# Optimization experiments

Measured on AMD Instinct MI355X. Metric: run time of the kernel, lower is better.

The kernel has to match this reference:

```python
import jax, jax.numpy as jnp
import numpy as np

N_NODES = 100000
N_EDGES = 1600000
IN_DIM = 256
HID_DIM = 64
NUM_CLASSES = 32
NEG_SLOPE = 0.01  # F.leaky_relu default


def setup_inputs() -> dict:
    key = jax.random.key(0)
    k1, k2, k3, k4, k5, k6 = jax.random.split(key, 6)
    return {
        "local_features": jax.random.normal(k1, (N_NODES, IN_DIM), dtype=jnp.float32),
        "edge_index": jax.random.randint(k2, (2, N_EDGES), 0, N_NODES, dtype=jnp.int64),
        "weight1": jax.random.uniform(k3, (IN_DIM, HID_DIM), dtype=jnp.float32),
        "weight2": jax.random.uniform(k4, (HID_DIM, NUM_CLASSES), dtype=jnp.float32),
        "att_weight1": jax.random.uniform(k5, (2 * HID_DIM, 1), dtype=jnp.float32),
        "att_weight2": jax.random.uniform(k6, (2 * NUM_CLASSES, 1), dtype=jnp.float32),
    }


def _gat_attention_aggregate(H, a, src, dst, n_nodes):
    # H: [N, D], a: [2D, 1]. Edge score = leaky_relu([H_src||H_dst] @ a)
    # computed without materializing [E, 2D]: split a into src/dst halves.
    d = H.shape[1]
    s_score = (H @ a[:d]).squeeze(-1)   # [N]
    d_score = (H @ a[d:]).squeeze(-1)   # [N]
    e = jax.nn.leaky_relu(s_score[src] + d_score[dst], NEG_SLOPE)  # [E]
    # segment softmax over each row (grouped by src), as torch.sparse.softmax(dim=1)
    m = jax.ops.segment_max(e, src, num_segments=n_nodes)          # [N]
    ex = jnp.exp(e - m[src])                                       # [E]
    denom = jax.ops.segment_sum(ex, src, num_segments=n_nodes)     # [N]
    att = ex / denom[src]                                          # [E]
    # sparse mm: out[i] = sum_{(i,j) in E} att_ij * H[j]
    return jax.ops.segment_sum(att[:, None] * H[dst], src, num_segments=n_nodes)


def reference(local_features, edge_index, weight1, weight2, att_weight1, att_weight2):
    src, dst = edge_index[0], edge_index[1]
    n = local_features.shape[0]
    Hw1 = local_features @ weight1                                  # [N, HID]
    hidden = jax.nn.elu(_gat_attention_aggregate(Hw1, att_weight1, src, dst, n))
    Hw2 = hidden @ weight2                                          # [N, C]
    out = _gat_attention_aggregate(Hw2, att_weight2, src, dst, n)
    return jax.nn.log_softmax(out, axis=1)
```

## Files before the change

kernel.cpp:

```cpp
#include <hip/hip_runtime.h>
#include <math.h>

#define IN_DIM 256
#define HID 64
#define NC 32
#define NEG 0.01f
#define INF_NEG -1e30f
#define SXR 68
#define MAXNBK 512
#define SLOT 8256
#define BCAP 12288
#define BIN_CHUNK 8192

static inline int ceil_div(int a, int b){ return (a + b - 1) / b; }

static __device__ __forceinline__ float lrelu(float x){ return x > 0.f ? x : NEG * x; }


__global__ __launch_bounds__(256) void bin_kernel(const int* __restrict__ src,
      const int* __restrict__ dst, int* __restrict__ cursor,
      unsigned int* __restrict__ tmp, int E, int nbk){
  __shared__ unsigned int payload[BIN_CHUNK];
  __shared__ unsigned short bid[BIN_CHUNK];
  __shared__ int cnt[MAXNBK];
  __shared__ int lofs[MAXNBK];
  __shared__ int gbase[MAXNBK];
  __shared__ int s2[256];
  int tid = threadIdx.x;
  int beg = blockIdx.x * BIN_CHUNK;
  int end = min(E, beg + BIN_CHUNK);
  int len = end - beg;

  for (int i = tid; i < MAXNBK; i += 256) cnt[i] = 0;
  __syncthreads();
  for (int e = beg + tid; e < end; e += 256)
    atomicAdd(&cnt[src[e] >> 8], 1);
  __syncthreads();
  int a0 = cnt[2 * tid], a1 = cnt[2 * tid + 1];
  int pair = a0 + a1;
  s2[tid] = pair; __syncthreads();
  int val = pair;
  for (int off = 1; off < 256; off <<= 1){
    int add = (tid >= off) ? s2[tid - off] : 0;
    __syncthreads();
    val += add; s2[tid] = val;
    __syncthreads();
  }
  int ep = val - pair;
  lofs[2 * tid] = ep;
  lofs[2 * tid + 1] = ep + a0;
  __syncthreads();
  for (int i = tid; i < nbk; i += 256){
    int c = cnt[i];
    gbase[i] = (c > 0) ? atomicAdd(&cursor[i], c) : 0;
  }
  __syncthreads();
  for (int i = tid; i < MAXNBK; i += 256) cnt[i] = 0;
  __syncthreads();
  for (int e = beg + tid; e < end; e += 256){
    int s = src[e];
    int b = s >> 8;
    int r = atomicAdd(&cnt[b], 1);
    int pos = lofs[b] + r;
    payload[pos] = ((unsigned)(s & 255) << 17) | (unsigned)dst[e];
    bid[pos] = (unsigned short)b;
  }
  __syncthreads();
  for (int pos = tid; pos < len; pos += 256){
    int b = bid[pos];
    int idx = pos - lofs[b];
    int g = gbase[b] + idx;
    if (g < SLOT) tmp[(size_t)b * SLOT + g] = payload[pos];
  }
}

__global__ __launch_bounds__(512) void bucket_base_kernel(const int* __restrict__ cursor,
      int* __restrict__ bbase, int nbk){
  __shared__ int sh[512];
  int tid = threadIdx.x;
  int v = (tid < nbk) ? min(cursor[tid], SLOT) : 0;
  sh[tid] = v; __syncthreads();
  int val = v;
  for (int off = 1; off < 512; off <<= 1){
    int add = (tid >= off) ? sh[tid - off] : 0;
    __syncthreads();
    val += add; sh[tid] = val;
    __syncthreads();
  }
  if (tid < nbk) bbase[tid] = val - v;
}

__global__ __launch_bounds__(256) void bucket_scatter_kernel(const unsigned int* __restrict__ tmp,
      const int* __restrict__ cursor, const int* __restrict__ bbase,
      int* __restrict__ row_ptr, int* __restrict__ csr, int n){
  __shared__ int cnt[256];
  __shared__ int cur[256];
  __shared__ int lbuf[BCAP];
  int tid = threadIdx.x;
  int b = blockIdx.x;
  int n0 = b << 8;
  int nn = min(256, n - n0);
  int len = min(cursor[b], SLOT);
  int segb = bbase[b];
  const unsigned int* T = tmp + (size_t)b * SLOT;
  cnt[tid] = 0;
  __syncthreads();
  for (int e = tid; e < len; e += 256) atomicAdd(&cnt[T[e] >> 17], 1);
  __syncthreads();
  int tv = cnt[tid];
  int val = tv;
  for (int off = 1; off < 256; off <<= 1){
    int add = (tid >= off) ? cnt[tid - off] : 0;
    __syncthreads();
    val += add; cnt[tid] = val;
    __syncthreads();
  }
  int excl = val - tv;
  cur[tid] = excl;
  if (tid < nn) row_ptr[n0 + tid] = segb + excl;
  if (n0 + nn == n && tid == 0) row_ptr[n] = segb + len;
  __syncthreads();
  if (len <= BCAP){
    for (int e = tid; e < len; e += 256){
      unsigned v = T[e];
      int pos = atomicAdd(&cur[v >> 17], 1);
      lbuf[pos] = (int)(v & 0x1FFFF);
    }
    __syncthreads();
    for (int e = tid; e < len; e += 256) csr[segb + e] = lbuf[e];
  } else {
    for (int e = tid; e < len; e += 256){
      unsigned v = T[e];
      int pos = atomicAdd(&cur[v >> 17], 1);
      csr[segb + pos] = (int)(v & 0x1FFFF);
    }
  }
}


__global__ void hist_kernel(const int* __restrict__ src, int* __restrict__ counts, int E){
  int i = blockIdx.x * blockDim.x + threadIdx.x;
  if (i < E) atomicAdd(&counts[src[i]], 1);
}
__global__ void scan_blocks_kernel(const int* __restrict__ counts, int* __restrict__ excl,
                                   int* __restrict__ bsums, int n){
  __shared__ int sh[256];
  int tid = threadIdx.x;
  int base = blockIdx.x * 1024 + tid * 4;
  int c[4]; int tsum = 0;
  #pragma unroll
  for (int j = 0; j < 4; j++){ int i = base + j; c[j] = (i < n) ? counts[i] : 0; tsum += c[j]; }
  sh[tid] = tsum; __syncthreads();
  int val = tsum;
  for (int off = 1; off < 256; off <<= 1){
    int add = (tid >= off) ? sh[tid - off] : 0;
    __syncthreads();
    val += add; sh[tid] = val;
    __syncthreads();
  }
  int p = val - tsum;
  #pragma unroll
  for (int j = 0; j < 4; j++){ int i = base + j; if (i < n) excl[i] = p; p += c[j]; }
  if (tid == 255) bsums[blockIdx.x] = val;
}
__global__ void scan_sums_kernel(int* __restrict__ bsums, int* __restrict__ row_ptr,
                                 int nb, int n, int E){
  __shared__ int sh[256];
  int tid = threadIdx.x;
  int v = (tid < nb) ? bsums[tid] : 0;
  sh[tid] = v; __syncthreads();
  int val = v;
  for (int off = 1; off < 256; off <<= 1){
    int add = (tid >= off) ? sh[tid - off] : 0;
    __syncthreads();
    val += add; sh[tid] = val;
    __syncthreads();
  }
  if (tid < nb) bsums[tid] = val - v;
  if (tid == 0) row_ptr[n] = E;
}
__global__ void add_offsets_kernel(int* __restrict__ excl, const int* __restrict__ bsums, int n){
  int i = blockIdx.x * 1024 + threadIdx.x;
  if (i < n) excl[i] += bsums[blockIdx.x];
}
__global__ void scatter_kernel(const int* __restrict__ src, const int* __restrict__ dst,
                               const int* __restrict__ row_ptr, int* __restrict__ fill,
                               int* __restrict__ csr, int E){
  int i = blockIdx.x * blockDim.x + threadIdx.x;
  if (i >= E) return;
  int s = src[i];
  int pos = row_ptr[s] + atomicAdd(&fill[s], 1);
  csr[pos] = dst[i];
}


__global__ __launch_bounds__(256) void gemm1_kernel(const float* __restrict__ X, const float* __restrict__ W,
      const float* __restrict__ a, float* __restrict__ H,
      float* __restrict__ svec, float* __restrict__ dvec, int n){
  __shared__ float xs[128 * SXR];
  __shared__ float ws[64 * 64];
  int tid = threadIdx.x;
  int r0 = blockIdx.x * 128;
  int tr = tid >> 4;
  int tc = tid & 15;
  int srow = tid >> 4, sc4 = tid & 15;

  float4 pfx[8], pfw[4];
  #pragma unroll
  for (int p = 0; p < 8; p++){
    int row = p * 16 + srow;
    int gr = r0 + row;
    pfx[p] = make_float4(0.f, 0.f, 0.f, 0.f);
    if (gr < n) pfx[p] = *(const float4*)(X + (size_t)gr * IN_DIM + sc4 * 4);
  }
  #pragma unroll
  for (int p = 0; p < 4; p++){
    int k = p * 16 + srow;
    pfw[p] = *(const float4*)(W + (size_t)k * 64 + sc4 * 4);
  }

  float acc[8][4];
  #pragma unroll
  for (int i = 0; i < 8; i++)
    #pragma unroll
    for (int j = 0; j < 4; j++) acc[i][j] = 0.f;

  for (int kb = 0; kb < 4; kb++){
    __syncthreads();
    #pragma unroll
    for (int p = 0; p < 8; p++){
      int row = p * 16 + srow;
      *(float4*)(xs + row * SXR + sc4 * 4) = pfx[p];
    }
    #pragma unroll
    for (int p = 0; p < 4; p++){
      int k = p * 16 + srow;
      *(float4*)(ws + k * 64 + sc4 * 4) = pfw[p];
    }
    if (kb < 3){
      #pragma unroll
      for (int p = 0; p < 8; p++){
        int row = p * 16 + srow;
        int gr = r0 + row;
        pfx[p] = make_float4(0.f, 0.f, 0.f, 0.f);
        if (gr < n) pfx[p] = *(const float4*)(X + (size_t)gr * IN_DIM + (kb + 1) * 64 + sc4 * 4);
      }
      #pragma unroll
      for (int p = 0; p < 4; p++){
        int k = p * 16 + srow;
        pfw[p] = *(const float4*)(W + (size_t)((kb + 1) * 64 + k) * 64 + sc4 * 4);
      }
    }
    __syncthreads();
    for (int kq = 0; kq < 16; kq++){
      float xr[8][4];
      #pragma unroll
      for (int i = 0; i < 8; i++){
        float4 v = *(const float4*)(xs + (tr * 8 + i) * SXR + kq * 4);
        xr[i][0] = v.x; xr[i][1] = v.y; xr[i][2] = v.z; xr[i][3] = v.w;
      }
      #pragma unroll
      for (int dk = 0; dk < 4; dk++){
        float4 w4 = *(const float4*)(ws + (size_t)(kq * 4 + dk) * 64 + tc * 4);
        float wv[4] = {w4.x, w4.y, w4.z, w4.w};
        #pragma unroll
        for (int i = 0; i < 8; i++)
          #pragma unroll
          for (int j = 0; j < 4; j++) acc[i][j] = fmaf(xr[i][dk], wv[j], acc[i][j]);
      }
    }
  }

  float av[4], bv[4];
  #pragma unroll
  for (int j = 0; j < 4; j++){ av[j] = a[tc * 4 + j]; bv[j] = a[64 + tc * 4 + j]; }
  float sp[8], dp[8];
  #pragma unroll
  for (int i = 0; i < 8; i++){
    float s = 0.f, d = 0.f;
    #pragma unroll
    for (int j = 0; j < 4; j++){ s = fmaf(acc[i][j], av[j], s); d = fmaf(acc[i][j], bv[j], d); }
    sp[i] = s; dp[i] = d;
  }
  #pragma unroll
  for (int off = 1; off < 16; off <<= 1){
    #pragma unroll
    for (int i = 0; i < 8; i++){
      sp[i] += __shfl_xor(sp[i], off, 16);
      dp[i] += __shfl_xor(dp[i], off, 16);
    }
  }
  #pragma unroll
  for (int i = 0; i < 8; i++){
    int r = r0 + tr * 8 + i;
    if (r < n){
      *(float4*)(H + (size_t)r * 64 + tc * 4) = make_float4(acc[i][0], acc[i][1], acc[i][2], acc[i][3]);
      if (tc == 0){ svec[r] = sp[i]; dvec[r] = dp[i]; }
    }
  }
}


__global__ __launch_bounds__(256) void gemm2_kernel(const float* __restrict__ X, const float* __restrict__ W,
      const float* __restrict__ a, float* __restrict__ H,
      float* __restrict__ svec, float* __restrict__ dvec, int n){
  __shared__ float xs[128 * SXR];
  __shared__ float ws[64 * 32];
  int tid = threadIdx.x;
  int r0 = blockIdx.x * 128;
  int tr = tid >> 4;
  int tc = tid & 15;
  int srow = tid >> 4, sc4 = tid & 15;

  #pragma unroll
  for (int p = 0; p < 8; p++){
    int row = p * 16 + srow;
    int gr = r0 + row;
    float4 v = make_float4(0.f, 0.f, 0.f, 0.f);
    if (gr < n) v = *(const float4*)(X + (size_t)gr * HID + sc4 * 4);
    *(float4*)(xs + row * SXR + sc4 * 4) = v;
  }
  #pragma unroll
  for (int p = 0; p < 2; p++){
    int idx = p * 256 + tid;
    int k = idx >> 3, c4 = idx & 7;
    *(float4*)(ws + k * 32 + c4 * 4) = *(const float4*)(W + (size_t)k * 32 + c4 * 4);
  }
  __syncthreads();

  float acc[8][2];
  #pragma unroll
  for (int i = 0; i < 8; i++){ acc[i][0] = 0.f; acc[i][1] = 0.f; }

  for (int kq = 0; kq < 16; kq++){
    float xr[8][4];
    #pragma unroll
    for (int i = 0; i < 8; i++){
      float4 v = *(const float4*)(xs + (tr * 8 + i) * SXR + kq * 4);
      xr[i][0] = v.x; xr[i][1] = v.y; xr[i][2] = v.z; xr[i][3] = v.w;
    }
    #pragma unroll
    for (int dk = 0; dk < 4; dk++){
      float2 w2 = *(const float2*)(ws + (size_t)(kq * 4 + dk) * 32 + tc * 2);
      #pragma unroll
      for (int i = 0; i < 8; i++){
        acc[i][0] = fmaf(xr[i][dk], w2.x, acc[i][0]);
        acc[i][1] = fmaf(xr[i][dk], w2.y, acc[i][1]);
      }
    }
  }

  float a0 = a[tc * 2], a1 = a[tc * 2 + 1];
  float b0 = a[32 + tc * 2], b1 = a[32 + tc * 2 + 1];
  float sp[8], dp[8];
  #pragma unroll
  for (int i = 0; i < 8; i++){
    sp[i] = fmaf(acc[i][0], a0, acc[i][1] * a1);
    dp[i] = fmaf(acc[i][0], b0, acc[i][1] * b1);
  }
  #pragma unroll
  for (int off = 1; off < 16; off <<= 1){
    #pragma unroll
    for (int i = 0; i < 8; i++){
      sp[i] += __shfl_xor(sp[i], off, 16);
      dp[i] += __shfl_xor(dp[i], off, 16);
    }
  }
  #pragma unroll
  for (int i = 0; i < 8; i++){
    int r = r0 + tr * 8 + i;
    if (r < n){
      *(float2*)(H + (size_t)r * NC + tc * 2) = make_float2(acc[i][0], acc[i][1]);
      if (tc == 0){ svec[r] = sp[i]; dvec[r] = dp[i]; }
    }
  }
}


__global__ __launch_bounds__(256) void agg1_kernel(const float* __restrict__ H, const float* __restrict__ sv,
      const float* __restrict__ dv, const int* __restrict__ row_ptr, const int* __restrict__ csr,
      float* __restrict__ out, int n){
  int t = blockIdx.x * 256 + threadIdx.x;
  int g = t >> 4, fl = t & 15;
  if (g >= n) return;
  int beg = row_ptr[g], end = row_ptr[g + 1];
  float si = sv[g];
  float m = INF_NEG, l = 0.f;
  float ox = 0.f, oy = 0.f, oz = 0.f, ow = 0.f;

  for (int cb = beg; cb < end; cb += 32){
    int ce = min(cb + 32, end);
    int e0 = cb + fl, e1 = cb + 16 + fl;
    int d0 = 0, d1 = 0;
    float ev0 = INF_NEG, ev1 = INF_NEG;
    if (e0 < ce){ d0 = csr[e0]; ev0 = lrelu(si + dv[d0]); }
    if (e1 < ce){ d1 = csr[e1]; ev1 = lrelu(si + dv[d1]); }
    float lm = fmaxf(ev0, ev1);
    #pragma unroll
    for (int off = 1; off < 16; off <<= 1) lm = fmaxf(lm, __shfl_xor(lm, off, 16));
    float nm = fmaxf(m, lm);
    float alpha = __expf(m - nm);
    m = nm;
    ev0 = __expf(ev0 - nm);
    ev1 = __expf(ev1 - nm);
    float ll = ev0 + ev1;
    #pragma unroll
    for (int off = 1; off < 16; off <<= 1) ll += __shfl_xor(ll, off, 16);
    l = l * alpha + ll;
    ox *= alpha; oy *= alpha; oz *= alpha; ow *= alpha;
    #pragma unroll
    for (int jj = 0; jj < 16; jj++){
      int e = cb + jj;
      if (e >= ce) break;
      float wgt = __shfl(ev0, jj, 16);
      int dd = __shfl(d0, jj, 16);
      float4 v = *(const float4*)(H + (size_t)dd * 64 + fl * 4);
      ox = fmaf(wgt, v.x, ox); oy = fmaf(wgt, v.y, oy);
      oz = fmaf(wgt, v.z, oz); ow = fmaf(wgt, v.w, ow);
    }
    #pragma unroll
    for (int jj = 0; jj < 16; jj++){
      int e = cb + 16 + jj;
      if (e >= ce) break;
      float wgt = __shfl(ev1, jj, 16);
      int dd = __shfl(d1, jj, 16);
      float4 v = *(const float4*)(H + (size_t)dd * 64 + fl * 4);
      ox = fmaf(wgt, v.x, ox); oy = fmaf(wgt, v.y, oy);
      oz = fmaf(wgt, v.z, oz); ow = fmaf(wgt, v.w, ow);
    }
  }
  float inv = (l > 0.f) ? 1.f / l : 0.f;
  ox *= inv; oy *= inv; oz *= inv; ow *= inv;
  ox = ox > 0.f ? ox : __expf(ox) - 1.f;
  oy = oy > 0.f ? oy : __expf(oy) - 1.f;
  oz = oz > 0.f ? oz : __expf(oz) - 1.f;
  ow = ow > 0.f ? ow : __expf(ow) - 1.f;
  *(float4*)(out + (size_t)g * 64 + fl * 4) = make_float4(ox, oy, oz, ow);
}


__global__ __launch_bounds__(256) void agg2_kernel(const float* __restrict__ H, const float* __restrict__ sv,
      const float* __restrict__ dv, const int* __restrict__ row_ptr, const int* __restrict__ csr,
      float* __restrict__ out, int n){
  int t = blockIdx.x * 256 + threadIdx.x;
  int g = t >> 3, fl = t & 7;
  if (g >= n) return;
  int beg = row_ptr[g], end = row_ptr[g + 1];
  float si = sv[g];
  float m = INF_NEG, l = 0.f;
  float ox = 0.f, oy = 0.f, oz = 0.f, ow = 0.f;

  for (int cb = beg; cb < end; cb += 32){
    int ce = min(cb + 32, end);
    float ev[4]; int dd4[4];
    float lm = INF_NEG;
    #pragma unroll
    for (int s = 0; s < 4; s++){
      int e = cb + s * 8 + fl;
      ev[s] = INF_NEG; dd4[s] = 0;
      if (e < ce){ dd4[s] = csr[e]; ev[s] = lrelu(si + dv[dd4[s]]); }
      lm = fmaxf(lm, ev[s]);
    }
    #pragma unroll
    for (int off = 1; off < 8; off <<= 1) lm = fmaxf(lm, __shfl_xor(lm, off, 8));
    float nm = fmaxf(m, lm);
    float alpha = __expf(m - nm);
    m = nm;
    float ll = 0.f;
    #pragma unroll
    for (int s = 0; s < 4; s++){ ev[s] = __expf(ev[s] - nm); ll += ev[s]; }
    #pragma unroll
    for (int off = 1; off < 8; off <<= 1) ll += __shfl_xor(ll, off, 8);
    l = l * alpha + ll;
    ox *= alpha; oy *= alpha; oz *= alpha; ow *= alpha;
    #pragma unroll
    for (int s = 0; s < 4; s++){
      #pragma unroll
      for (int jj = 0; jj < 8; jj++){
        int e = cb + s * 8 + jj;
        if (e >= ce) break;
        float wgt = __shfl(ev[s], jj, 8);
        int dd = __shfl(dd4[s], jj, 8);
        float4 v = *(const float4*)(H + (size_t)dd * 32 + fl * 4);
        ox = fmaf(wgt, v.x, ox); oy = fmaf(wgt, v.y, oy);
        oz = fmaf(wgt, v.z, oz); ow = fmaf(wgt, v.w, ow);
      }
    }
  }
  float inv = (l > 0.f) ? 1.f / l : 0.f;
  ox *= inv; oy *= inv; oz *= inv; ow *= inv;
  float tm = fmaxf(fmaxf(ox, oy), fmaxf(oz, ow));
  #pragma unroll
  for (int off = 1; off < 8; off <<= 1) tm = fmaxf(tm, __shfl_xor(tm, off, 8));
  float se = __expf(ox - tm) + __expf(oy - tm) + __expf(oz - tm) + __expf(ow - tm);
  #pragma unroll
  for (int off = 1; off < 8; off <<= 1) se += __shfl_xor(se, off, 8);
  float lg = tm + __logf(se);
  *(float4*)(out + (size_t)g * 32 + fl * 4) = make_float4(ox - lg, oy - lg, oz - lg, ow - lg);
}


extern "C" void kernel_launch(void* const* d_in, const int* in_sizes, int n_in,
                              void* d_out, int out_size, void* d_ws, size_t ws_size,
                              hipStream_t stream) {
  (void)n_in; (void)out_size; (void)ws_size;
  const float* X  = (const float*)d_in[0];
  const int*   EI = (const int*)d_in[1];
  const float* W1 = (const float*)d_in[2];
  const float* W2 = (const float*)d_in[3];
  const float* A1 = (const float*)d_in[4];
  const float* A2 = (const float*)d_in[5];
  float* out = (float*)d_out;

  int N = in_sizes[0] / IN_DIM;
  int E = in_sizes[1] / 2;
  const int* src = EI;
  const int* dst = EI + E;

  auto align_up = [](size_t x){ return (x + 511) & ~(size_t)511; };
  char* w = (char*)d_ws;
  int* counts  = (int*)w;   w += align_up((size_t)N * 4);
  int* cursor  = (int*)w;   w += align_up((size_t)MAXNBK * 4);
  int* bbase   = (int*)w;   w += align_up((size_t)MAXNBK * 4);
  int* row_ptr = (int*)w;   w += align_up((size_t)(N + 1) * 4);
  int* bsums   = (int*)w;   w += align_up(1024);
  int* csr     = (int*)w;   w += align_up((size_t)E * 4);
  float* H1    = (float*)w; w += align_up((size_t)N * 64 * 4);
  float* hid   = (float*)w; w += align_up((size_t)N * 64 * 4);
  float* s1    = (float*)w; w += align_up((size_t)N * 4);
  float* d1    = (float*)w; w += align_up((size_t)N * 4);
  float* s2    = (float*)w; w += align_up((size_t)N * 4);
  float* d2    = (float*)w; w += align_up((size_t)N * 4);
  float* H2    = H1;
  unsigned int* tmp = (unsigned int*)hid;

  int nbk = ceil_div(N, 256);

  if (N <= (1 << 17) && nbk <= MAXNBK && (size_t)nbk * SLOT <= (size_t)N * 64){
    hipMemsetAsync(cursor, 0, (size_t)nbk * 4, stream);
    bin_kernel<<<ceil_div(E, BIN_CHUNK), 256, 0, stream>>>(src, dst, cursor, tmp, E, nbk);
    bucket_base_kernel<<<1, 512, 0, stream>>>(cursor, bbase, nbk);
    bucket_scatter_kernel<<<nbk, 256, 0, stream>>>(tmp, cursor, bbase, row_ptr, csr, N);
  } else {
    int nb = ceil_div(N, 1024);
    hipMemsetAsync(counts, 0, (size_t)N * 4, stream);
    hist_kernel<<<ceil_div(E, 256), 256, 0, stream>>>(src, counts, E);
    scan_blocks_kernel<<<nb, 256, 0, stream>>>(counts, row_ptr, bsums, N);
    scan_sums_kernel<<<1, 256, 0, stream>>>(bsums, row_ptr, nb, N, E);
    add_offsets_kernel<<<nb, 1024, 0, stream>>>(row_ptr, bsums, N);
    hipMemsetAsync(counts, 0, (size_t)N * 4, stream);
    scatter_kernel<<<ceil_div(E, 256), 256, 0, stream>>>(src, dst, row_ptr, counts, csr, E);
  }

  gemm1_kernel<<<ceil_div(N, 128), 256, 0, stream>>>(X, W1, A1, H1, s1, d1, N);
  agg1_kernel<<<ceil_div(N * 16, 256), 256, 0, stream>>>(H1, s1, d1, row_ptr, csr, hid, N);
  gemm2_kernel<<<ceil_div(N, 128), 256, 0, stream>>>(hid, W2, A2, H2, s2, d2, N);
  agg2_kernel<<<ceil_div(N * 8, 256), 256, 0, stream>>>(H2, s2, d2, row_ptr, csr, out, N);
}
```

Measured before the change: 390.8 us.

## Use wavefront-per-node aggregation, fold bucket scan into scatter, shrink gemm1 k-tile

The aggregation kernels now give each node a full 64-lane wavefront instead of a 16- or 8-lane group. Lanes load 64 edges at once and split the neighbor gathers across sub-groups, then combine partial sums with cross-lane shuffles. The separate bucket-base scan kernel is removed; each scatter block instead sums the preceding bucket counts itself, which saves a launch at the cost of redundant reads. gemm1 moves to 32-wide k tiles with smaller shared memory, aiming for higher occupancy but needing more barrier iterations.

```diff
diff --git a/kernel.cpp b/kernel.cpp
--- a/kernel.cpp
+++ b/kernel.cpp
@@ -7,6 +7,7 @@
 #define NEG 0.01f
 #define INF_NEG -1e30f
 #define SXR 68
+#define SB 36
 #define MAXNBK 512
 #define SLOT 8256
 #define BCAP 12288
@@ -74,34 +75,27 @@
   }
 }
 
-__global__ __launch_bounds__(512) void bucket_base_kernel(const int* __restrict__ cursor,
-      int* __restrict__ bbase, int nbk){
-  __shared__ int sh[512];
-  int tid = threadIdx.x;
-  int v = (tid < nbk) ? min(cursor[tid], SLOT) : 0;
-  sh[tid] = v; __syncthreads();
-  int val = v;
-  for (int off = 1; off < 512; off <<= 1){
-    int add = (tid >= off) ? sh[tid - off] : 0;
-    __syncthreads();
-    val += add; sh[tid] = val;
-    __syncthreads();
-  }
-  if (tid < nbk) bbase[tid] = val - v;
-}
-
 __global__ __launch_bounds__(256) void bucket_scatter_kernel(const unsigned int* __restrict__ tmp,
-      const int* __restrict__ cursor, const int* __restrict__ bbase,
-      int* __restrict__ row_ptr, int* __restrict__ csr, int n){
+      const int* __restrict__ cursor, int* __restrict__ row_ptr, int* __restrict__ csr,
+      int n, int nbk){
+  __shared__ int red[256];
   __shared__ int cnt[256];
   __shared__ int cur[256];
   __shared__ int lbuf[BCAP];
   int tid = threadIdx.x;
   int b = blockIdx.x;
+  int partial = 0;
+  for (int i = tid; i < b; i += 256) partial += min(cursor[i], SLOT);
+  red[tid] = partial;
+  __syncthreads();
+  for (int s = 128; s > 0; s >>= 1){
+    if (tid < s) red[tid] += red[tid + s];
+    __syncthreads();
+  }
+  int segb = red[0];
   int n0 = b << 8;
   int nn = min(256, n - n0);
   int len = min(cursor[b], SLOT);
-  int segb = bbase[b];
   const unsigned int* T = tmp + (size_t)b * SLOT;
   cnt[tid] = 0;
   __syncthreads();
@@ -197,26 +191,27 @@
 __global__ __launch_bounds__(256) void gemm1_kernel(const float* __restrict__ X, const float* __restrict__ W,
       const float* __restrict__ a, float* __restrict__ H,
       float* __restrict__ svec, float* __restrict__ dvec, int n){
-  __shared__ float xs[128 * SXR];
-  __shared__ float ws[64 * 64];
+  __shared__ float xs[128 * SB];
+  __shared__ float ws[32 * 64];
   int tid = threadIdx.x;
   int r0 = blockIdx.x * 128;
   int tr = tid >> 4;
   int tc = tid & 15;
-  int srow = tid >> 4, sc4 = tid & 15;
-
-  float4 pfx[8], pfw[4];
-  #pragma unroll
-  for (int p = 0; p < 8; p++){
-    int row = p * 16 + srow;
+
+  float4 pfx[4]; float4 pfw[2];
+  #pragma unroll
+  for (int p = 0; p < 4; p++){
+    int idx = p * 256 + tid;
+    int row = idx >> 3, c8 = idx & 7;
     int gr = r0 + row;
     pfx[p] = make_float4(0.f, 0.f, 0.f, 0.f);
-    if (gr < n) pfx[p] = *(const float4*)(X + (size_t)gr * IN_DIM + sc4 * 4);
-  }
-  #pragma unroll
-  for (int p = 0; p < 4; p++){
-    int k = p * 16 + srow;
-    pfw[p] = *(const float4*)(W + (size_t)k * 64 + sc4 * 4);
+    if (gr < n) pfx[p] = *(const float4*)(X + (size_t)gr * IN_DIM + c8 * 4);
+  }
+  #pragma unroll
+  for (int p = 0; p < 2; p++){
+    int idx = p * 256 + tid;
+    int k = idx >> 4, c4 = idx & 15;
+    pfw[p] = *(const float4*)(W + (size_t)k * 64 + c4 * 4);
   }
 
   float acc[8][4];
@@ -225,38 +220,42 @@
     #pragma unroll
     for (int j = 0; j < 4; j++) acc[i][j] = 0.f;
 
-  for (int kb = 0; kb < 4; kb++){
-    __syncthreads();
-    #pragma unroll
-    for (int p = 0; p < 8; p++){
-      int row = p * 16 + srow;
-      *(float4*)(xs + row * SXR + sc4 * 4) = pfx[p];
-    }
+  for (int kb = 0; kb < 8; kb++){
+    __syncthreads();
     #pragma unroll
     for (int p = 0; p < 4; p++){
-      int k = p * 16 + srow;
-      *(float4*)(ws + k * 64 + sc4 * 4) = pfw[p];
-    }
-    if (kb < 3){
+      int idx = p * 256 + tid;
+      int row = idx >> 3, c8 = idx & 7;
+      *(float4*)(xs + row * SB + c8 * 4) = pfx[p];
+    }
+    #pragma unroll
+    for (int p = 0; p < 2; p++){
+      int idx = p * 256 + tid;
+      int k = idx >> 4, c4 = idx & 15;
+      *(float4*)(ws + k * 64 + c4 * 4) = pfw[p];
+    }
+    if (kb < 7){
       #pragma unroll
-      for (int p = 0; p < 8; p++){
-        int row = p * 16 + srow;
+      for (int p = 0; p < 4; p++){
+        int idx = p * 256 + tid;
+        int row = idx >> 3, c8 = idx & 7;
         int gr = r0 + row;
         pfx[p] = make_float4(0.f, 0.f, 0.f, 0.f);
-        if (gr < n) pfx[p] = *(const float4*)(X + (size_t)gr * IN_DIM + (kb + 1) * 64 + sc4 * 4);
+        if (gr < n) pfx[p] = *(const float4*)(X + (size_t)gr * IN_DIM + (kb + 1) * 32 + c8 * 4);
       }
       #pragma unroll
-      for (int p = 0; p < 4; p++){
-        int k = p * 16 + srow;
-        pfw[p] = *(const float4*)(W + (size_t)((kb + 1) * 64 + k) * 64 + sc4 * 4);
-      }
-    }
-    __syncthreads();
-    for (int kq = 0; kq < 16; kq++){
+      for (int p = 0; p < 2; p++){
+        int idx = p * 256 + tid;
+        int k = idx >> 4, c4 = idx & 15;
+        pfw[p] = *(const float4*)(W + (size_t)((kb + 1) * 32 + k) * 64 + c4 * 4);
+      }
+    }
+    __syncthreads();
+    for (int kq = 0; kq < 8; kq++){
       float xr[8][4];
       #pragma unroll
       for (int i = 0; i < 8; i++){
-        float4 v = *(const float4*)(xs + (tr * 8 + i) * SXR + kq * 4);
+        float4 v = *(const float4*)(xs + (tr * 8 + i) * SB + kq * 4);
         xr[i][0] = v.x; xr[i][1] = v.y; xr[i][2] = v.z; xr[i][3] = v.w;
       }
       #pragma unroll
@@ -380,113 +379,104 @@
 __global__ __launch_bounds__(256) void agg1_kernel(const float* __restrict__ H, const float* __restrict__ sv,
       const float* __restrict__ dv, const int* __restrict__ row_ptr, const int* __restrict__ csr,
       float* __restrict__ out, int n){
-  int t = blockIdx.x * 256 + threadIdx.x;
-  int g = t >> 4, fl = t & 15;
+  int g = (blockIdx.x * 256 + threadIdx.x) >> 6;
   if (g >= n) return;
+  int lane = threadIdx.x & 63;
+  int sub = lane >> 4, fl = lane & 15;
   int beg = row_ptr[g], end = row_ptr[g + 1];
   float si = sv[g];
   float m = INF_NEG, l = 0.f;
   float ox = 0.f, oy = 0.f, oz = 0.f, ow = 0.f;
 
-  for (int cb = beg; cb < end; cb += 32){
-    int ce = min(cb + 32, end);
-    int e0 = cb + fl, e1 = cb + 16 + fl;
-    int d0 = 0, d1 = 0;
-    float ev0 = INF_NEG, ev1 = INF_NEG;
-    if (e0 < ce){ d0 = csr[e0]; ev0 = lrelu(si + dv[d0]); }
-    if (e1 < ce){ d1 = csr[e1]; ev1 = lrelu(si + dv[d1]); }
-    float lm = fmaxf(ev0, ev1);
-    #pragma unroll
-    for (int off = 1; off < 16; off <<= 1) lm = fmaxf(lm, __shfl_xor(lm, off, 16));
+  for (int cb = beg; cb < end; cb += 64){
+    int cnt = min(64, end - cb);
+    int dd = 0; float ev = INF_NEG;
+    if (lane < cnt){ dd = csr[cb + lane]; ev = lrelu(si + dv[dd]); }
+    float lm = ev;
+    #pragma unroll
+    for (int off = 1; off < 64; off <<= 1) lm = fmaxf(lm, __shfl_xor(lm, off, 64));
     float nm = fmaxf(m, lm);
     float alpha = __expf(m - nm);
     m = nm;
-    ev0 = __expf(ev0 - nm);
-    ev1 = __expf(ev1 - nm);
-    float ll = ev0 + ev1;
-    #pragma unroll
-    for (int off = 1; off < 16; off <<= 1) ll += __shfl_xor(ll, off, 16);
+    float wgt = __expf(ev - nm);
+    float ll = wgt;
+    #pragma unroll
+    for (int off = 1; off < 64; off <<= 1) ll += __shfl_xor(ll, off, 64);
     l = l * alpha + ll;
     ox *= alpha; oy *= alpha; oz *= alpha; ow *= alpha;
-    #pragma unroll
-    for (int jj = 0; jj < 16; jj++){
-      int e = cb + jj;
-      if (e >= ce) break;
-      float wgt = __shfl(ev0, jj, 16);
-      int dd = __shfl(d0, jj, 16);
-      float4 v = *(const float4*)(H + (size_t)dd * 64 + fl * 4);
-      ox = fmaf(wgt, v.x, ox); oy = fmaf(wgt, v.y, oy);
-      oz = fmaf(wgt, v.z, oz); ow = fmaf(wgt, v.w, ow);
-    }
-    #pragma unroll
-    for (int jj = 0; jj < 16; jj++){
-      int e = cb + 16 + jj;
-      if (e >= ce) break;
-      float wgt = __shfl(ev1, jj, 16);
-      int dd = __shfl(d1, jj, 16);
-      float4 v = *(const float4*)(H + (size_t)dd * 64 + fl * 4);
-      ox = fmaf(wgt, v.x, ox); oy = fmaf(wgt, v.y, oy);
-      oz = fmaf(wgt, v.z, oz); ow = fmaf(wgt, v.w, ow);
-    }
-  }
+    int trips = (cnt + 3) >> 2;
+    for (int t = 0; t < trips; t++){
+      int j = t * 4 + sub;
+      int js = min(j, cnt - 1);
+      float wj = __shfl(wgt, js, 64);
+      int dj = __shfl(dd, js, 64);
+      if (j < cnt){
+        float4 v = *(const float4*)(H + (size_t)dj * 64 + fl * 4);
+        ox = fmaf(wj, v.x, ox); oy = fmaf(wj, v.y, oy);
+        oz = fmaf(wj, v.z, oz); ow = fmaf(wj, v.w, ow);
+      }
+    }
+  }
+  ox += __shfl_xor(ox, 16, 64); ox += __shfl_xor(ox, 32, 64);
+  oy += __shfl_xor(oy, 16, 64); oy += __shfl_xor(oy, 32, 64);
+  oz += __shfl_xor(oz, 16, 64); oz += __shfl_xor(oz, 32, 64);
+  ow += __shfl_xor(ow, 16, 64); ow += __shfl_xor(ow, 32, 64);
   float inv = (l > 0.f) ? 1.f / l : 0.f;
   ox *= inv; oy *= inv; oz *= inv; ow *= inv;
   ox = ox > 0.f ? ox : __expf(ox) - 1.f;
   oy = oy > 0.f ? oy : __expf(oy) - 1.f;
   oz = oz > 0.f ? oz : __expf(oz) - 1.f;
   ow = ow > 0.f ? ow : __expf(ow) - 1.f;
-  *(float4*)(out + (size_t)g * 64 + fl * 4) = make_float4(ox, oy, oz, ow);
+  if (sub == 0)
+    *(float4*)(out + (size_t)g * 64 + fl * 4) = make_float4(ox, oy, oz, ow);
 }
 
 
 __global__ __launch_bounds__(256) void agg2_kernel(const float* __restrict__ H, const float* __restrict__ sv,
       const float* __restrict__ dv, const int* __restrict__ row_ptr, const int* __restrict__ csr,
       float* __restrict__ out, int n){
-  int t = blockIdx.x * 256 + threadIdx.x;
-  int g = t >> 3, fl = t & 7;
+  int g = (blockIdx.x * 256 + threadIdx.x) >> 6;
   if (g >= n) return;
+  int lane = threadIdx.x & 63;
+  int sub = lane >> 3, fl = lane & 7;
   int beg = row_ptr[g], end = row_ptr[g + 1];
   float si = sv[g];
   float m = INF_NEG, l = 0.f;
   float ox = 0.f, oy = 0.f, oz = 0.f, ow = 0.f;
 
-  for (int cb = beg; cb < end; cb += 32){
-    int ce = min(cb + 32, end);
-    float ev[4]; int dd4[4];
-    float lm = INF_NEG;
-    #pragma unroll
-    for (int s = 0; s < 4; s++){
-      int e = cb + s * 8 + fl;
-      ev[s] = INF_NEG; dd4[s] = 0;
-      if (e < ce){ dd4[s] = csr[e]; ev[s] = lrelu(si + dv[dd4[s]]); }
-      lm = fmaxf(lm, ev[s]);
-    }
-    #pragma unroll
-    for (int off = 1; off < 8; off <<= 1) lm = fmaxf(lm, __shfl_xor(lm, off, 8));
+  for (int cb = beg; cb < end; cb += 64){
+    int cnt = min(64, end - cb);
+    int dd = 0; float ev = INF_NEG;
+    if (lane < cnt){ dd = csr[cb + lane]; ev = lrelu(si + dv[dd]); }
+    float lm = ev;
+    #pragma unroll
+    for (int off = 1; off < 64; off <<= 1) lm = fmaxf(lm, __shfl_xor(lm, off, 64));
     float nm = fmaxf(m, lm);
     float alpha = __expf(m - nm);
     m = nm;
-    float ll = 0.f;
-    #pragma unroll
-    for (int s = 0; s < 4; s++){ ev[s] = __expf(ev[s] - nm); ll += ev[s]; }
-    #pragma unroll
-    for (int off = 1; off < 8; off <<= 1) ll += __shfl_xor(ll, off, 8);
+    float wgt = __expf(ev - nm);
+    float ll = wgt;
+    #pragma unroll
+    for (int off = 1; off < 64; off <<= 1) ll += __shfl_xor(ll, off, 64);
     l = l * alpha + ll;
     ox *= alpha; oy *= alpha; oz *= alpha; ow *= alpha;
-    #pragma unroll
-    for (int s = 0; s < 4; s++){
-      #pragma unroll
-      for (int jj = 0; jj < 8; jj++){
-        int e = cb + s * 8 + jj;
-        if (e >= ce) break;
-        float wgt = __shfl(ev[s], jj, 8);
-        int dd = __shfl(dd4[s], jj, 8);
-        float4 v = *(const float4*)(H + (size_t)dd * 32 + fl * 4);
-        ox = fmaf(wgt, v.x, ox); oy = fmaf(wgt, v.y, oy);
-        oz = fmaf(wgt, v.z, oz); ow = fmaf(wgt, v.w, ow);
-      }
-    }
-  }
+    int trips = (cnt + 7) >> 3;
+    for (int t = 0; t < trips; t++){
+      int j = t * 8 + sub;
+      int js = min(j, cnt - 1);
+      float wj = __shfl(wgt, js, 64);
+      int dj = __shfl(dd, js, 64);
+      if (j < cnt){
+        float4 v = *(const float4*)(H + (size_t)dj * 32 + fl * 4);
+        ox = fmaf(wj, v.x, ox); oy = fmaf(wj, v.y, oy);
+        oz = fmaf(wj, v.z, oz); ow = fmaf(wj, v.w, ow);
+      }
+    }
+  }
+  ox += __shfl_xor(ox, 8, 64); ox += __shfl_xor(ox, 16, 64); ox += __shfl_xor(ox, 32, 64);
+  oy += __shfl_xor(oy, 8, 64); oy += __shfl_xor(oy, 16, 64); oy += __shfl_xor(oy, 32, 64);
+  oz += __shfl_xor(oz, 8, 64); oz += __shfl_xor(oz, 16, 64); oz += __shfl_xor(oz, 32, 64);
+  ow += __shfl_xor(ow, 8, 64); ow += __shfl_xor(ow, 16, 64); ow += __shfl_xor(ow, 32, 64);
   float inv = (l > 0.f) ? 1.f / l : 0.f;
   ox *= inv; oy *= inv; oz *= inv; ow *= inv;
   float tm = fmaxf(fmaxf(ox, oy), fmaxf(oz, ow));
@@ -496,7 +486,8 @@
   #pragma unroll
   for (int off = 1; off < 8; off <<= 1) se += __shfl_xor(se, off, 8);
   float lg = tm + __logf(se);
-  *(float4*)(out + (size_t)g * 32 + fl * 4) = make_float4(ox - lg, oy - lg, oz - lg, ow - lg);
+  if (sub == 0)
+    *(float4*)(out + (size_t)g * 32 + fl * 4) = make_float4(ox - lg, oy - lg, oz - lg, ow - lg);
 }
 
 
@@ -521,7 +512,6 @@
   char* w = (char*)d_ws;
   int* counts  = (int*)w;   w += align_up((size_t)N * 4);
   int* cursor  = (int*)w;   w += align_up((size_t)MAXNBK * 4);
-  int* bbase   = (int*)w;   w += align_up((size_t)MAXNBK * 4);
   int* row_ptr = (int*)w;   w += align_up((size_t)(N + 1) * 4);
   int* bsums   = (int*)w;   w += align_up(1024);
   int* csr     = (int*)w;   w += align_up((size_t)E * 4);
@@ -539,8 +529,7 @@
   if (N <= (1 << 17) && nbk <= MAXNBK && (size_t)nbk * SLOT <= (size_t)N * 64){
     hipMemsetAsync(cursor, 0, (size_t)nbk * 4, stream);
     bin_kernel<<<ceil_div(E, BIN_CHUNK), 256, 0, stream>>>(src, dst, cursor, tmp, E, nbk);
-    bucket_base_kernel<<<1, 512, 0, stream>>>(cursor, bbase, nbk);
-    bucket_scatter_kernel<<<nbk, 256, 0, stream>>>(tmp, cursor, bbase, row_ptr, csr, N);
+    bucket_scatter_kernel<<<nbk, 256, 0, stream>>>(tmp, cursor, row_ptr, csr, N, nbk);
   } else {
     int nb = ceil_div(N, 1024);
     hipMemsetAsync(counts, 0, (size_t)N * 4, stream);
@@ -553,7 +542,7 @@
   }
 
   gemm1_kernel<<<ceil_div(N, 128), 256, 0, stream>>>(X, W1, A1, H1, s1, d1, N);
-  agg1_kernel<<<ceil_div(N * 16, 256), 256, 0, stream>>>(H1, s1, d1, row_ptr, csr, hid, N);
+  agg1_kernel<<<ceil_div(N, 4), 256, 0, stream>>>(H1, s1, d1, row_ptr, csr, hid, N);
   gemm2_kernel<<<ceil_div(N, 128), 256, 0, stream>>>(hid, W2, A2, H2, s2, d2, N);
-  agg2_kernel<<<ceil_div(N * 8, 256), 256, 0, stream>>>(H2, s2, d2, row_ptr, csr, out, N);
-}
+  agg2_kernel<<<ceil_div(N, 4), 256, 0, stream>>>(H2, s2, d2, row_ptr, csr, out, N);
+}
```

Measured after the change: 396.4 us. No clear change (+1.4%).
